# Optimization experiments

Hardware: AMD Instinct MI355X
Metric: run time of the kernel (lower is better)

The kernel has to match this reference:

```python
import jax, jax.numpy as jnp
import numpy as np

H = 200          # GRU hidden size (hard-coded in module)
D = 300          # embed_dim
V = 50000        # embed_num (vocab)
DOC_TRUNC = 10
N_DOCS = 256
T = 50           # words per sentence


def _p(k, shape):
    return jax.random.normal(k, shape, dtype=jnp.float32) * 0.05


def setup_inputs():
    key = jax.random.key(0)
    ks = jax.random.split(key, 24)
    x = jax.random.randint(ks[0], (N_DOCS * DOC_TRUNC, T), 0, V, dtype=jnp.int32)
    doc_lens = jax.random.randint(ks[1], (N_DOCS,), 0, DOC_TRUNC + 1, dtype=jnp.int32)
    emb = _p(ks[2], (V, D)).at[0].set(0.0)  # padding_idx=0 row is zero
    inp = dict(
        x=x, doc_nums=N_DOCS, doc_lens=doc_lens, emb=emb,
        wf_ih=_p(ks[3], (3 * H, D)), wf_hh=_p(ks[4], (3 * H, H)), wf_bi=_p(ks[5], (3 * H,)), wf_bh=_p(ks[6], (3 * H,)),
        wb_ih=_p(ks[7], (3 * H, D)), wb_hh=_p(ks[8], (3 * H, H)), wb_bi=_p(ks[9], (3 * H,)), wb_bh=_p(ks[10], (3 * H,)),
        sf_ih=_p(ks[11], (3 * H, 2 * H)), sf_hh=_p(ks[12], (3 * H, H)), sf_bi=_p(ks[13], (3 * H,)), sf_bh=_p(ks[14], (3 * H,)),
        sb_ih=_p(ks[15], (3 * H, 2 * H)), sb_hh=_p(ks[16], (3 * H, H)), sb_bi=_p(ks[17], (3 * H,)), sb_bh=_p(ks[18], (3 * H,)),
        doc_w=_p(ks[19], (1, 2 * H)), doc_b=_p(ks[20], (1,)),
        sent_w=_p(ks[21], (DOC_TRUNC, 2 * H)), sent_b=_p(ks[22], (DOC_TRUNC,)),
    )
    return inp


def _gru_dir(xseq, w_ih, w_hh, b_ih, b_hh, reverse=False):
    # xseq: [B, T, Din] -> outputs [B, T, H], torch GRU gate order (r, z, n)
    if reverse:
        xseq = xseq[:, ::-1]
    gx = jnp.einsum('btd,gd->btg', xseq, w_ih) + b_ih  # [B, T, 3H]
    gx = jnp.moveaxis(gx, 1, 0)                        # [T, B, 3H]
    h0 = jnp.zeros((xseq.shape[0], H), xseq.dtype)

    def step(h, gxt):
        gh = h @ w_hh.T + b_hh
        xr, xz, xn = jnp.split(gxt, 3, axis=-1)
        hr, hz, hn = jnp.split(gh, 3, axis=-1)
        r = jax.nn.sigmoid(xr + hr)
        z = jax.nn.sigmoid(xz + hz)
        n = jnp.tanh(xn + r * hn)
        h_new = (1.0 - z) * n + z * h
        return h_new, h_new

    _, hs = jax.lax.scan(step, h0, gx)
    hs = jnp.moveaxis(hs, 0, 1)  # [B, T, H]
    if reverse:
        hs = hs[:, ::-1]
    return hs


def _bigru(xseq, fw, bw):
    return jnp.concatenate([_gru_dir(xseq, *fw), _gru_dir(xseq, *bw, reverse=True)], axis=-1)


def _avg_pool(xseq, lens):
    # Faithful to max_pool1d helper: avg over first lens[i] timesteps, zeros if len==0.
    Tn = xseq.shape[1]
    mask = (jnp.arange(Tn)[None, :] < lens[:, None]).astype(xseq.dtype)  # [B, T]
    s = jnp.einsum('btf,bt->bf', xseq, mask)
    denom = jnp.maximum(lens, 1).astype(xseq.dtype)[:, None]
    return jnp.where((lens == 0)[:, None], jnp.zeros_like(s), s / denom)


def reference(x, doc_nums, doc_lens, emb,
              wf_ih, wf_hh, wf_bi, wf_bh, wb_ih, wb_hh, wb_bi, wb_bh,
              sf_ih, sf_hh, sf_bi, sf_bh, sb_ih, sb_hh, sb_bi, sb_bh,
              doc_w, doc_b, sent_w, sent_b):
    sent_lens = jnp.sum(jnp.sign(x), axis=1)                 # [B_sent]
    e = emb[x]                                               # [B_sent, T, D]
    hw = _bigru(e, (wf_ih, wf_hh, wf_bi, wf_bh), (wb_ih, wb_hh, wb_bi, wb_bh))  # [B_sent, T, 2H]
    s = _avg_pool(hw, sent_lens)                             # [B_sent, 2H]
    s = s.reshape(-1, DOC_TRUNC, 2 * H)                      # [N_docs, doc_trunc, 2H]
    hs = _bigru(s, (sf_ih, sf_hh, sf_bi, sf_bh), (sb_ih, sb_hh, sb_bi, sb_bh))  # [N_docs, doc_trunc, 2H]
    d = _avg_pool(hs, doc_lens)                              # [N_docs, 2H]
    doc_pro = (d @ doc_w.T + doc_b).reshape(-1)              # [N_docs]
    sent_pro = d @ sent_w.T + sent_b                         # [N_docs, doc_trunc]
    dl = np.asarray(doc_lens)                                # concrete index data (static)
    rows = np.repeat(np.arange(dl.shape[0]), dl)
    cols = np.concatenate([np.arange(int(l)) for l in dl]).astype(np.int32) if rows.size else np.zeros((0,), np.int32)
    target = jnp.concatenate([doc_pro, sent_pro[rows, cols]])
    return jax.nn.sigmoid(target)
```

## Files before the change

kernel.cpp:

```cpp
#include <hip/hip_runtime.h>
#include <hip/hip_bf16.h>


typedef __hip_bfloat16 bf16;
typedef _Float16 h16x8 __attribute__((ext_vector_type(8)));
typedef __fp16 fp16x2 __attribute__((ext_vector_type(2)));
typedef float f32x4 __attribute__((ext_vector_type(4)));

#define HDIM 200
#define NS   2560
#define TW   50
#define ND   256
#define DTR  10
#define VEMB 50000

#define GT   13
#define NT   39
#define NTP  40
#define KCH  7
#define HSTR 232
#define KC_W 10
#define KC_S 13

__device__ __forceinline__ float sigf(float x) {
    return __builtin_amdgcn_rcpf(1.f + __expf(-x));
}
__device__ __forceinline__ float tanh_fast(float x) {
    float e = __expf(2.f * x);
    return (e - 1.f) * __builtin_amdgcn_rcpf(e + 1.f);
}
__device__ __forceinline__ unsigned short f2h(float x) {
    union { _Float16 h; unsigned short u; } v;
    v.h = (_Float16)x;
    return v.u;
}
__device__ __forceinline__ float h2f(unsigned short u) {
    union { _Float16 h; unsigned short u; } v;
    v.u = u;
    return (float)v.h;
}
__device__ __forceinline__ unsigned pk2h(float a, float b) {
    union { fp16x2 p; unsigned u; } v;
    v.p = __builtin_amdgcn_cvt_pkrtz(a, b);
    return v.u;
}
__device__ __forceinline__ float hfsel(uint2 v, int rg) {
    unsigned u = (rg & 2) ? v.y : v.x;
    return h2f((unsigned short)((rg & 1) ? (u >> 16) : (u & 0xFFFFu)));
}

#define PB_EMBH 12500
#define PB_WHH  (PB_EMBH + 273)
#define PB_BIH  (PB_WHH + 460)
#define PB_ALL  (PB_BIH + 20)

__global__ void prepack_all(
    const float* __restrict__ emb, unsigned short* __restrict__ embH,
    const float* __restrict__ whh0, const float* __restrict__ whh1,
    const float* __restrict__ whh2, const float* __restrict__ whh3,
    unsigned short* __restrict__ Bhh,
    const float* __restrict__ wih0, const float* __restrict__ wih1,
    const float* __restrict__ wih2, const float* __restrict__ wih3,
    unsigned short* __restrict__ BiW0, unsigned short* __restrict__ BiW1,
    unsigned short* __restrict__ BiS0, unsigned short* __restrict__ BiS1,
    const int* __restrict__ x, int* __restrict__ sl,
    const float* bi0, const float* bh0, const float* bi1, const float* bh1,
    const float* bi2, const float* bh2, const float* bi3, const float* bh3,
    float* __restrict__ bt)
{
    const int b = blockIdx.x;
    const int tid = threadIdx.x;

    if (b < PB_EMBH) {
        int gid = b * 256 + tid;
        int row = gid >> 6, c = gid & 63;
        if (c >= 40) return;
        int k0 = c * 8;
        unsigned short vals[8] __attribute__((aligned(16)));
        if (k0 + 7 < 300) {
            const float4 f0 = *reinterpret_cast<const float4*>(emb + (size_t)row * 300 + k0);
            const float4 f1 = *reinterpret_cast<const float4*>(emb + (size_t)row * 300 + k0 + 4);
            unsigned u0 = pk2h(f0.x, f0.y), u1 = pk2h(f0.z, f0.w);
            unsigned u2 = pk2h(f1.x, f1.y), u3 = pk2h(f1.z, f1.w);
            vals[0] = (unsigned short)u0; vals[1] = (unsigned short)(u0 >> 16);
            vals[2] = (unsigned short)u1; vals[3] = (unsigned short)(u1 >> 16);
            vals[4] = (unsigned short)u2; vals[5] = (unsigned short)(u2 >> 16);
            vals[6] = (unsigned short)u3; vals[7] = (unsigned short)(u3 >> 16);
        } else {
#pragma unroll
            for (int jj = 0; jj < 8; ++jj) {
                int k = k0 + jj;
                vals[jj] = (k < 300) ? f2h(emb[(size_t)row * 300 + k]) : (unsigned short)0;
            }
        }
        *reinterpret_cast<uint4*>(embH + (size_t)row * 320 + k0) =
            *reinterpret_cast<const uint4*>(vals);
        return;
    }

    if (b < PB_WHH) {
        int gid = (b - PB_EMBH) * 256 + tid;
        if (gid >= 4 * NT * KCH * 64) return;
        int lane = gid & 63;
        int f = gid >> 6;
        int kc = f % KCH;
        int tIdx = (f / KCH) % NT;
        int d = f / (KCH * NT);
        const float* w = (d == 0) ? whh0 : (d == 1) ? whh1 : (d == 2) ? whh2 : whh3;
        int g = tIdx / GT, j = tIdx % GT;
        int il = j * 16 + (lane & 15);
        int n = g * HDIM + il;
        int kb = kc * 32 + (lane >> 4) * 8;
        unsigned short vals[8] __attribute__((aligned(16)));
#pragma unroll
        for (int jj = 0; jj < 8; ++jj) {
            int k = kb + jj;
            float v = (il < HDIM && k < HDIM) ? w[n * HDIM + k] : 0.f;
            vals[jj] = f2h(v);
        }
        *reinterpret_cast<float4*>(reinterpret_cast<char*>(Bhh) + (size_t)gid * 16) =
            *reinterpret_cast<const float4*>(vals);
        return;
    }

    if (b < PB_BIH) {
        int rel = b - PB_WHH;
        const float* w; unsigned short* Bp; int Kin, KC, base;
        if (rel < 100)      { w = wih0; Bp = BiW0; Kin = 300; KC = KC_W; base = 0; }
        else if (rel < 200) { w = wih1; Bp = BiW1; Kin = 300; KC = KC_W; base = 100; }
        else if (rel < 330) { w = wih2; Bp = BiS0; Kin = 400; KC = KC_S; base = 200; }
        else                { w = wih3; Bp = BiS1; Kin = 400; KC = KC_S; base = 330; }
        int gid = (rel - base) * 256 + tid;
        if (gid >= NTP * KC * 64) return;
        int lane = gid & 63;
        int f = gid >> 6;
        int kc = f % KC;
        int tIdx = f / KC;
        int g = tIdx / GT, j = tIdx % GT;
        int il = j * 16 + (lane & 15);
        int n = g * HDIM + il;
        int kb = kc * 32 + (lane >> 4) * 8;
        unsigned short vals[8] __attribute__((aligned(16)));
#pragma unroll
        for (int jj = 0; jj < 8; ++jj) {
            int k = kb + jj;
            float v = (tIdx < NT && il < HDIM && k < Kin) ? w[n * Kin + k] : 0.f;
            vals[jj] = f2h(v);
        }
        *reinterpret_cast<float4*>(reinterpret_cast<char*>(Bp) + (size_t)gid * 16) =
            *reinterpret_cast<const float4*>(vals);
        return;
    }

    {
        int gid = (b - PB_BIH) * 256 + tid;
        if (gid < NS) {
            int c = 0;
            for (int t = 0; t < TW; ++t) c += (x[gid * TW + t] != 0) ? 1 : 0;
            sl[gid] = c;
            return;
        }
        int g2 = gid - NS;
        if (g2 >= 4 * 624) return;
        int d = g2 / 624, col = g2 % 624;
        int g = col / 208, i = col % 208;
        const float* bi = (d == 0) ? bi0 : (d == 1) ? bi1 : (d == 2) ? bi2 : bi3;
        const float* bh = (d == 0) ? bh0 : (d == 1) ? bh1 : (d == 2) ? bh2 : bh3;
        float v = 0.f;
        if (i < HDIM) v = (g < 2) ? (bi[g * HDIM + i] + bh[g * HDIM + i]) : bi[2 * HDIM + i];
        bt[g2] = v;
    }
}

__global__ __launch_bounds__(512, 2) void gemm_word_fused(
    const unsigned short* __restrict__ embH, const int* __restrict__ idx,
    const unsigned short* __restrict__ Bp0, const unsigned short* __restrict__ Bp1,
    const float* __restrict__ bt0, const float* __restrict__ bt1,
    unsigned short* __restrict__ gx0, unsigned short* __restrict__ gx1,
    int nF, int t0F, int t0B)
{
    __shared__ __align__(16) unsigned short As[128 * 320];

    const int tid = threadIdx.x;
    const int wv = tid >> 6, lane = tid & 63;
    const int d = (blockIdx.x >= nF) ? 1 : 0;
    const int bm = d ? (blockIdx.x - nF) : blockIdx.x;
    const unsigned short* Bp = d ? Bp1 : Bp0;
    const float* bt = d ? bt1 : bt0;
    unsigned short* gxOut = d ? gx1 : gx0;
    const int t0 = d ? t0B : t0F;
    const int m_w = wv & 1, n_w = wv >> 1;

    {
        const int srow = tid >> 2, qk = tid & 3;
        int rp = bm * 128 + srow;
        int tok = idx[(rp % NS) * TW + (rp / NS) + t0];
        const unsigned short* src = embH + (size_t)tok * 320 + qk * 8;
        uint4 v[KC_W];
#pragma unroll
        for (int kc = 0; kc < KC_W; ++kc)
            v[kc] = *reinterpret_cast<const uint4*>(src + kc * 32);
        const int rx = srow & 7;
        unsigned short* dst = &As[srow * 320];
#pragma unroll
        for (int kc = 0; kc < KC_W; ++kc) {
            int slot = (kc * 4 + qk) ^ rx;
            *reinterpret_cast<uint4*>(dst + slot * 8) = v[kc];
        }
    }
    __syncthreads();

    f32x4 acc[4][10];
#pragma unroll
    for (int i = 0; i < 4; ++i)
#pragma unroll
        for (int j = 0; j < 10; ++j) acc[i][j] = (f32x4){0.f, 0.f, 0.f, 0.f};

    const uint4* bq = reinterpret_cast<const uint4*>(Bp);
    const int q = lane >> 4;
    int abase[4], arx[4];
#pragma unroll
    for (int mt = 0; mt < 4; ++mt) {
        int row = m_w * 64 + mt * 16 + (lane & 15);
        abase[mt] = row * 320;
        arx[mt] = row & 7;
    }

#pragma unroll 2
    for (int kc = 0; kc < KC_W; ++kc) {
        h16x8 ah[4];
#pragma unroll
        for (int mt = 0; mt < 4; ++mt) {
            int slot = (kc * 4 + q) ^ arx[mt];
            ah[mt] = *reinterpret_cast<const h16x8*>(&As[abase[mt] + slot * 8]);
        }
#pragma unroll
        for (int half = 0; half < 2; ++half) {
            uint4 b[5];
#pragma unroll
            for (int j = 0; j < 5; ++j) {
                int gnt = n_w * 10 + half * 5 + j;
                b[j] = bq[(size_t)(gnt * KC_W + kc) * 64 + lane];
            }
#pragma unroll
            for (int mt = 0; mt < 4; ++mt)
#pragma unroll
                for (int j = 0; j < 5; ++j)
                    acc[mt][half * 5 + j] = __builtin_amdgcn_mfma_f32_16x16x32_f16(
                        ah[mt], *reinterpret_cast<const h16x8*>(&b[j]),
                        acc[mt][half * 5 + j], 0, 0, 0);
        }
    }

    float btv[10];
#pragma unroll
    for (int j = 0; j < 10; ++j) {
        int gnt = n_w * 10 + j;
        btv[j] = (gnt < NT) ? bt[gnt * 16 + (lane & 15)] : 0.f;
    }

#pragma unroll
    for (int mt = 0; mt < 4; ++mt) {
        int gmt = bm * 8 + m_w * 4 + mt;
#pragma unroll
        for (int j = 0; j < 10; ++j) {
            int gnt = n_w * 10 + j;
            if (gnt < NT) {
                uint2 v;
                v.x = pk2h(acc[mt][j][0] + btv[j], acc[mt][j][1] + btv[j]);
                v.y = pk2h(acc[mt][j][2] + btv[j], acc[mt][j][3] + btv[j]);
                *reinterpret_cast<uint2*>(reinterpret_cast<char*>(gxOut) +
                    ((size_t)(gmt * NT + gnt) * 64 + lane) * 8) = v;
            }
        }
    }
}

__global__ __launch_bounds__(512, 2) void gemm_sent(
    const float* __restrict__ Afl, int astride,
    const unsigned short* __restrict__ Bp0, const unsigned short* __restrict__ Bp1,
    const float* __restrict__ bt0, const float* __restrict__ bt1,
    unsigned short* __restrict__ gx0, unsigned short* __restrict__ gx1, int nF)
{
    __shared__ __align__(16) unsigned short As[2][128 * 32];

    const int tid = threadIdx.x;
    const int wv = tid >> 6, lane = tid & 63;
    const int d = (blockIdx.x >= nF) ? 1 : 0;
    const int bm = d ? (blockIdx.x - nF) : blockIdx.x;
    const unsigned short* Bp = d ? Bp1 : Bp0;
    const float* bt = d ? bt1 : bt0;
    unsigned short* gxOut = d ? gx1 : gx0;
    const int m_w = wv & 1, n_w = wv >> 1;

    int aaddr[4];
#pragma unroll
    for (int mt = 0; mt < 4; ++mt) {
        int row = m_w * 64 + mt * 16 + (lane & 15);
        aaddr[mt] = row * 32 + (((lane >> 4) ^ ((row >> 1) & 3)) << 3);
    }

    const int srow = tid >> 2, qk = tid & 3;
    const int ssw = (srow >> 1) & 3;

    f32x4 acc[4][10];
#pragma unroll
    for (int i = 0; i < 4; ++i)
#pragma unroll
        for (int j = 0; j < 10; ++j) acc[i][j] = (f32x4){0.f, 0.f, 0.f, 0.f};

    const uint4* bq = reinterpret_cast<const uint4*>(Bp);
    const float* arow = Afl + (size_t)(bm * 128 + srow) * astride + qk * 8;

    float4 f[2], fn[2];
#pragma unroll
    for (int j = 0; j < 2; ++j)
        f[j] = *reinterpret_cast<const float4*>(arow + j * 4);

    for (int kc = 0; kc < KC_S; ++kc) {
        unsigned short* Ab = &As[kc & 1][0];
        {
            uint4 vh;
            vh.x = pk2h(f[0].x, f[0].y);
            vh.y = pk2h(f[0].z, f[0].w);
            vh.z = pk2h(f[1].x, f[1].y);
            vh.w = pk2h(f[1].z, f[1].w);
            int slot = qk ^ ssw;
            *reinterpret_cast<uint4*>(&Ab[srow * 32 + slot * 8]) = vh;
        }
        __syncthreads();

        if (kc + 1 < KC_S) {
#pragma unroll
            for (int j = 0; j < 2; ++j)
                fn[j] = *reinterpret_cast<const float4*>(arow + (kc + 1) * 32 + j * 4);
        }

        h16x8 ah[4];
#pragma unroll
        for (int mt = 0; mt < 4; ++mt)
            ah[mt] = *reinterpret_cast<const h16x8*>(&Ab[aaddr[mt]]);

#pragma unroll
        for (int half = 0; half < 2; ++half) {
            uint4 b[5];
#pragma unroll
            for (int j = 0; j < 5; ++j) {
                int gnt = n_w * 10 + half * 5 + j;
                b[j] = bq[(size_t)(gnt * KC_S + kc) * 64 + lane];
            }
#pragma unroll
            for (int mt = 0; mt < 4; ++mt)
#pragma unroll
                for (int j = 0; j < 5; ++j)
                    acc[mt][half * 5 + j] = __builtin_amdgcn_mfma_f32_16x16x32_f16(
                        ah[mt], *reinterpret_cast<const h16x8*>(&b[j]),
                        acc[mt][half * 5 + j], 0, 0, 0);
        }
        if (kc + 1 < KC_S) { f[0] = fn[0]; f[1] = fn[1]; }
    }

    float btv[10];
#pragma unroll
    for (int j = 0; j < 10; ++j) {
        int gnt = n_w * 10 + j;
        btv[j] = (gnt < NT) ? bt[gnt * 16 + (lane & 15)] : 0.f;
    }

#pragma unroll
    for (int mt = 0; mt < 4; ++mt) {
        int gmt = bm * 8 + m_w * 4 + mt;
#pragma unroll
        for (int j = 0; j < 10; ++j) {
            int gnt = n_w * 10 + j;
            if (gnt < NT) {
                uint2 v;
                v.x = pk2h(acc[mt][j][0] + btv[j], acc[mt][j][1] + btv[j]);
                v.y = pk2h(acc[mt][j][2] + btv[j], acc[mt][j][3] + btv[j]);
                *reinterpret_cast<uint2*>(reinterpret_cast<char*>(gxOut) +
                    ((size_t)(gmt * NT + gnt) * 64 + lane) * 8) = v;
            }
        }
    }
}

__global__ __launch_bounds__(832) void gru_fused(
    const unsigned short* __restrict__ gxA, const unsigned short* __restrict__ gxB,
    const unsigned short* __restrict__ Bp, int dirBase0, int dirBase1,
    const float* __restrict__ bh0, const float* __restrict__ bh1,
    const int* __restrict__ lens, float* __restrict__ pool,
    int S, int T, int tSteps, int t0A, int t0B, int poolMode, int nF,
    int first, int last, unsigned short* __restrict__ hstate)
{
    __shared__ __align__(16) unsigned short hh[2][16 * HSTR];

    const int dsel = (blockIdx.x >= nF) ? 1 : 0;
    const int lb = dsel ? (blockIdx.x - nF) : blockIdx.x;
    const unsigned short* gx = dsel ? gxB : gxA;
    const int dirBase = dsel ? dirBase1 : dirBase0;
    const float* bh = dsel ? bh1 : bh0;
    const int dirOff = dsel ? HDIM : 0;
    const int rev = dsel;
    const int t0 = dsel ? t0B : t0A;

    const int tid = threadIdx.x;
    const int w = tid >> 6, lane = tid & 63;
    const int quad = lane >> 4, c = lane & 15;
    const int row0 = lb * 16;
    const int i = w * 16 + c;
    const bool iv = (i < HDIM);

    for (int p = tid; p < 16 * HSTR; p += 832) { hh[0][p] = 0; hh[1][p] = 0; }
    __syncthreads();

    const float bhn = iv ? bh[2 * HDIM + i] : 0.f;

    int slen[4];
    float hreg[4], pacc[4];
#pragma unroll
    for (int rg = 0; rg < 4; ++rg) {
        int L = lens[row0 + quad * 4 + rg];
        if (L < 0) L = 0;
        if (L > T) L = T;
        slen[rg] = L;
        hreg[rg] = 0.f; pacc[rg] = 0.f;
    }

    if (!first && iv) {
#pragma unroll
        for (int rg = 0; rg < 4; ++rg) {
            int sg = row0 + quad * 4 + rg;
            unsigned short hu = hstate[((size_t)dsel * NS + sg) * HDIM + i];
            hreg[rg] = h2f(hu);
            hh[0][(quad * 4 + rg) * HSTR + i] = hu;
        }
    }

    const float4* Bq = reinterpret_cast<const float4*>(Bp);
    h16x8 bfr[3][7];
#pragma unroll
    for (int g = 0; g < 3; ++g)
#pragma unroll
        for (int kc = 0; kc < KCH; ++kc) {
            int fidx = (dirBase + g * GT + w) * KCH + kc;
            float4 raw = Bq[(size_t)fidx * 64 + lane];
            bfr[g][kc] = *reinterpret_cast<h16x8*>(&raw);
        }

    const char* gxb = reinterpret_cast<const char*>(gx);
    const int am = c * HSTR + quad * 8;
    const int SG = S >> 4;
    const int hw0 = (quad * 4) * HSTR + i;
    const long long dstep = (long long)(rev ? -SG : SG) * NT * 512;
    __syncthreads();

    uint2 gxv[3], gnx[3];
    long long goff[3];
    {
        const int tl0 = rev ? (tSteps - 1) : 0;
        const long long gg = (long long)tl0 * SG + lb;
#pragma unroll
        for (int g = 0; g < 3; ++g) {
            long long off = ((gg * NT + g * GT + w) * 64 + lane) * 8;
            gxv[g] = *reinterpret_cast<const uint2*>(gxb + off);
            goff[g] = off + dstep;
        }
    }

    for (int ts = 0; ts < tSteps; ++ts) {
        const int t = rev ? (t0 + tSteps - 1 - ts) : (t0 + ts);
        const int cur = ts & 1, nxt = cur ^ 1;

        if (ts + 1 < tSteps) {
#pragma unroll
            for (int g = 0; g < 3; ++g) {
                gnx[g] = *reinterpret_cast<const uint2*>(gxb + goff[g]);
                goff[g] += dstep;
            }
        }

        f32x4 a0 = (f32x4){0.f, 0.f, 0.f, 0.f}, a1 = a0, a2 = a0;
#pragma unroll
        for (int kc = 0; kc < KCH; ++kc) {
            h16x8 ah = *reinterpret_cast<const h16x8*>(&hh[cur][am + kc * 32]);
            a0 = __builtin_amdgcn_mfma_f32_16x16x32_f16(ah, bfr[0][kc], a0, 0, 0, 0);
            a1 = __builtin_amdgcn_mfma_f32_16x16x32_f16(ah, bfr[1][kc], a1, 0, 0, 0);
            a2 = __builtin_amdgcn_mfma_f32_16x16x32_f16(ah, bfr[2][kc], a2, 0, 0, 0);
        }

        if (iv) {
#pragma unroll
            for (int rg = 0; rg < 4; ++rg) {
                float xr = hfsel(gxv[0], rg);
                float xz = hfsel(gxv[1], rg);
                float xn = hfsel(gxv[2], rg);
                float r = sigf(xr + a0[rg]);
                float z = sigf(xz + a1[rg]);
                float n = tanh_fast(xn + r * (a2[rg] + bhn));
                float hnew = n + z * (hreg[rg] - n);
                hreg[rg] = hnew;
                hh[nxt][hw0 + rg * HSTR] = f2h(hnew);
                pacc[rg] += (t < slen[rg]) ? hnew : 0.f;
            }
        }
        __syncthreads();
        if (ts + 1 < tSteps) {
#pragma unroll
            for (int g = 0; g < 3; ++g) gxv[g] = gnx[g];
        }
    }

    if (iv) {
#pragma unroll
        for (int rg = 0; rg < 4; ++rg) {
            int sg = row0 + quad * 4 + rg;
            if (!last) hstate[((size_t)dsel * NS + sg) * HDIM + i] = f2h(hreg[rg]);
            int L = slen[rg];
            float v = (L > 0) ? pacc[rg] / (float)L : 0.f;
            int prow = poolMode ? ((sg % 10) * ND + sg / 10) : sg;
            float* pp = &pool[(size_t)prow * 400 + dirOff + i];
            if (first) *pp = v; else *pp += v;
        }
    }
}

__global__ __launch_bounds__(64) void head_kernel(
    const float* __restrict__ d_pool, const int* __restrict__ doc_lens,
    const float* __restrict__ doc_w, const float* __restrict__ doc_b,
    const float* __restrict__ sent_w, const float* __restrict__ sent_b,
    float* __restrict__ out)
{
    const int d = blockIdx.x;
    const int lane = threadIdx.x;

    int part = 0;
#pragma unroll
    for (int rep = 0; rep < 4; ++rep) {
        int j = lane + rep * 64;
        int v = doc_lens[j];
        v = (v < 0) ? 0 : (v > DTR ? DTR : v);
        if (j < d) part += v;
    }
#pragma unroll
    for (int off = 32; off; off >>= 1) part += __shfl_down(part, off);
    int soff = __shfl(part, 0);

    int dl = doc_lens[d];
    dl = (dl < 0) ? 0 : (dl > DTR ? DTR : dl);
    const float* dv = d_pool + (size_t)d * 400;

    for (int o = 0; o <= dl; ++o) {
        const float* wrow = (o == 0) ? doc_w : sent_w + (o - 1) * 400;
        float s = 0.f;
        for (int f = lane; f < 400; f += 64) s += dv[f] * wrow[f];
#pragma unroll
        for (int off = 32; off; off >>= 1) s += __shfl_down(s, off);
        if (lane == 0) {
            float bias = (o == 0) ? doc_b[0] : sent_b[o - 1];
            out[(o == 0) ? d : (ND + soff + (o - 1))] = sigf(s + bias);
        }
    }
}

extern "C" void kernel_launch(void* const* d_in, const int* in_sizes, int n_in,
                              void* d_out, int out_size, void* d_ws, size_t ws_size,
                              hipStream_t stream) {
    const int*   x        = (const int*)d_in[0];
    const int*   doc_lens = (const int*)d_in[2];
    const float* emb      = (const float*)d_in[3];
    const float* wf_ih = (const float*)d_in[4];
    const float* wf_hh = (const float*)d_in[5];
    const float* wf_bi = (const float*)d_in[6];
    const float* wf_bh = (const float*)d_in[7];
    const float* wb_ih = (const float*)d_in[8];
    const float* wb_hh = (const float*)d_in[9];
    const float* wb_bi = (const float*)d_in[10];
    const float* wb_bh = (const float*)d_in[11];
    const float* sf_ih = (const float*)d_in[12];
    const float* sf_hh = (const float*)d_in[13];
    const float* sf_bi = (const float*)d_in[14];
    const float* sf_bh = (const float*)d_in[15];
    const float* sb_ih = (const float*)d_in[16];
    const float* sb_hh = (const float*)d_in[17];
    const float* sb_bi = (const float*)d_in[18];
    const float* sb_bh = (const float*)d_in[19];
    const float* doc_w  = (const float*)d_in[20];
    const float* doc_b  = (const float*)d_in[21];
    const float* sent_w = (const float*)d_in[22];
    const float* sent_b = (const float*)d_in[23];

    const size_t GXSZ   = 159744000;
    const size_t GXHALF = 79872000;
    const size_t HSSZ   = 2048000;
    char* ws = (char*)d_ws;
    const size_t base = GXSZ;
    const bool chunked = (ws_size == 0) || (ws_size >= base + 39528448 + HSSZ);

    unsigned short* gxF = (unsigned short*)(ws);
    unsigned short* gxB = (unsigned short*)(ws + GXHALF);
    unsigned short* gxS0 = (unsigned short*)(ws);
    unsigned short* gxS1 = (unsigned short*)(ws + 8000000);
    float* s_in   = (float*)(ws + base);
    float* dpool  = (float*)(ws + base + 4096256);
    int*   sl     = (int*)(ws + base + 4096256 + 409600);
    unsigned short* Bhh  = (unsigned short*)(ws + base + 4096256 + 409600 + 10240);
    unsigned short* BiW0 = (unsigned short*)((char*)Bhh + 1118208);
    unsigned short* BiW1 = BiW0 + NTP * KC_W * 64 * 8;
    unsigned short* BiS0 = (unsigned short*)((char*)BiW0 + 819200);
    unsigned short* BiS1 = BiS0 + NTP * KC_S * 64 * 8;
    float* bt     = (float*)((char*)BiS0 + 1064960);
    unsigned short* embH = (unsigned short*)((char*)bt + 9984);
    unsigned short* hstate = (unsigned short*)(ws + base + 39528448);

    prepack_all<<<PB_ALL, 256, 0, stream>>>(
        emb, embH,
        wf_hh, wb_hh, sf_hh, sb_hh, Bhh,
        wf_ih, wb_ih, sf_ih, sb_ih, BiW0, BiW1, BiS0, BiS1,
        x, sl,
        wf_bi, wf_bh, wb_bi, wb_bh, sf_bi, sf_bh, sb_bi, sb_bh, bt);

    if (chunked) {
        gemm_word_fused<<<1000, 512, 0, stream>>>(
            embH, x, BiW0, BiW1, bt + 0, bt + 624, gxF, gxB, 500, 0, 25);
        gru_fused<<<320, 832, 0, stream>>>(
            gxF, gxB, Bhh, 0 * NT, 1 * NT, wf_bh, wb_bh, sl, s_in,
            NS, TW, 25, 0, 25, 1, 160, 1, 0, hstate);
        gemm_word_fused<<<1000, 512, 0, stream>>>(
            embH, x, BiW0, BiW1, bt + 0, bt + 624, gxF, gxB, 500, 25, 0);
        gru_fused<<<320, 832, 0, stream>>>(
            gxF, gxB, Bhh, 0 * NT, 1 * NT, wf_bh, wb_bh, sl, s_in,
            NS, TW, 25, 25, 0, 1, 160, 0, 1, hstate);
    } else {
        gemm_word_fused<<<1000, 512, 0, stream>>>(
            embH, x, BiW0, BiW1, bt + 0, bt + 624, gxF, gxF, 1000, 0, 0);
        gru_fused<<<160, 832, 0, stream>>>(
            gxF, gxF, Bhh, 0 * NT, 1 * NT, wf_bh, wb_bh, sl, s_in,
            NS, TW, TW, 0, 0, 1, 160, 1, 1, hstate);
        gemm_word_fused<<<1000, 512, 0, stream>>>(
            embH, x, BiW0, BiW1, bt + 0, bt + 624, gxF, gxF, 0, 0, 0);
        gru_fused<<<160, 832, 0, stream>>>(
            gxF, gxF, Bhh, 0 * NT, 1 * NT, wf_bh, wb_bh, sl, s_in,
            NS, TW, TW, 0, 0, 1, 0, 1, 1, hstate);
    }

    gemm_sent<<<40, 512, 0, stream>>>(
        s_in, 400, BiS0, BiS1, bt + 2 * 624, bt + 3 * 624, gxS0, gxS1, 20);
    gru_fused<<<32, 832, 0, stream>>>(
        gxS0, gxS1, Bhh, 2 * NT, 3 * NT, sf_bh, sb_bh, doc_lens, dpool,
        ND, DTR, DTR, 0, 0, 0, 16, 1, 1, hstate);

    head_kernel<<<ND, 64, 0, stream>>>(dpool, doc_lens, doc_w, doc_b, sent_w, sent_b, (float*)d_out);
}
```

Before: 669.3 us.

## Drop time-chunked word GRU path and hstate carry; use int offsets

Removes the two-chunk word-level schedule, which ran two half-length projection GEMMs, each followed by a GRU launch running both directions. It also removes the fp16 hidden-state save and restore between chunks. Instead, one full-length GEMM and 50-step GRU run for the forward direction, then again for the backward direction. The GRU kernel loses its chunk parameters, writes the pool directly, switches gx addressing from 64-bit to 32-bit offsets, and asks for a minimum of 4 blocks per CU in launch bounds. This removes the hidden-state traffic and read-modify-write pooling, but serialises the two directions and doubles the per-launch recurrence length. The tighter launch bound also risks register spills.

```diff
diff --git a/kernel.cpp b/kernel.cpp
--- a/kernel.cpp
+++ b/kernel.cpp
@@ -384,13 +384,12 @@
     }
 }
 
-__global__ __launch_bounds__(832) void gru_fused(
+__global__ __launch_bounds__(832, 4) void gru_fused(
     const unsigned short* __restrict__ gxA, const unsigned short* __restrict__ gxB,
     const unsigned short* __restrict__ Bp, int dirBase0, int dirBase1,
     const float* __restrict__ bh0, const float* __restrict__ bh1,
     const int* __restrict__ lens, float* __restrict__ pool,
-    int S, int T, int tSteps, int t0A, int t0B, int poolMode, int nF,
-    int first, int last, unsigned short* __restrict__ hstate)
+    int S, int T, int poolMode, int nF)
 {
     __shared__ __align__(16) unsigned short hh[2][16 * HSTR];
 
@@ -401,7 +400,6 @@
     const float* bh = dsel ? bh1 : bh0;
     const int dirOff = dsel ? HDIM : 0;
     const int rev = dsel;
-    const int t0 = dsel ? t0B : t0A;
 
     const int tid = threadIdx.x;
     const int w = tid >> 6, lane = tid & 63;
@@ -426,16 +424,6 @@
         hreg[rg] = 0.f; pacc[rg] = 0.f;
     }
 
-    if (!first && iv) {
-#pragma unroll
-        for (int rg = 0; rg < 4; ++rg) {
-            int sg = row0 + quad * 4 + rg;
-            unsigned short hu = hstate[((size_t)dsel * NS + sg) * HDIM + i];
-            hreg[rg] = h2f(hu);
-            hh[0][(quad * 4 + rg) * HSTR + i] = hu;
-        }
-    }
-
     const float4* Bq = reinterpret_cast<const float4*>(Bp);
     h16x8 bfr[3][7];
 #pragma unroll
@@ -451,32 +439,30 @@
     const int am = c * HSTR + quad * 8;
     const int SG = S >> 4;
     const int hw0 = (quad * 4) * HSTR + i;
-    const long long dstep = (long long)(rev ? -SG : SG) * NT * 512;
+    const int GSTR = GT * 64 * 8;
+    const int dstep = (rev ? -SG : SG) * NT * 512;
     __syncthreads();
 
     uint2 gxv[3], gnx[3];
-    long long goff[3];
+    int boff;
     {
-        const int tl0 = rev ? (tSteps - 1) : 0;
-        const long long gg = (long long)tl0 * SG + lb;
-#pragma unroll
-        for (int g = 0; g < 3; ++g) {
-            long long off = ((gg * NT + g * GT + w) * 64 + lane) * 8;
-            gxv[g] = *reinterpret_cast<const uint2*>(gxb + off);
-            goff[g] = off + dstep;
-        }
-    }
-
-    for (int ts = 0; ts < tSteps; ++ts) {
-        const int t = rev ? (t0 + tSteps - 1 - ts) : (t0 + ts);
+        const int t0 = rev ? (T - 1) : 0;
+        boff = (((t0 * SG + lb) * NT + w) * 64 + lane) * 8;
+#pragma unroll
+        for (int g = 0; g < 3; ++g)
+            gxv[g] = *reinterpret_cast<const uint2*>(gxb + boff + g * GSTR);
+        boff += dstep;
+    }
+
+    for (int ts = 0; ts < T; ++ts) {
+        const int t = rev ? (T - 1 - ts) : ts;
         const int cur = ts & 1, nxt = cur ^ 1;
 
-        if (ts + 1 < tSteps) {
-#pragma unroll
-            for (int g = 0; g < 3; ++g) {
-                gnx[g] = *reinterpret_cast<const uint2*>(gxb + goff[g]);
-                goff[g] += dstep;
-            }
+        if (ts + 1 < T) {
+#pragma unroll
+            for (int g = 0; g < 3; ++g)
+                gnx[g] = *reinterpret_cast<const uint2*>(gxb + boff + g * GSTR);
+            boff += dstep;
         }
 
         f32x4 a0 = (f32x4){0.f, 0.f, 0.f, 0.f}, a1 = a0, a2 = a0;
@@ -504,7 +490,7 @@
             }
         }
         __syncthreads();
-        if (ts + 1 < tSteps) {
+        if (ts + 1 < T) {
 #pragma unroll
             for (int g = 0; g < 3; ++g) gxv[g] = gnx[g];
         }
@@ -514,12 +500,10 @@
 #pragma unroll
         for (int rg = 0; rg < 4; ++rg) {
             int sg = row0 + quad * 4 + rg;
-            if (!last) hstate[((size_t)dsel * NS + sg) * HDIM + i] = f2h(hreg[rg]);
             int L = slen[rg];
             float v = (L > 0) ? pacc[rg] / (float)L : 0.f;
             int prow = poolMode ? ((sg % 10) * ND + sg / 10) : sg;
-            float* pp = &pool[(size_t)prow * 400 + dirOff + i];
-            if (first) *pp = v; else *pp += v;
+            pool[(size_t)prow * 400 + dirOff + i] = v;
         }
     }
 }
@@ -589,15 +573,11 @@
     const float* sent_w = (const float*)d_in[22];
     const float* sent_b = (const float*)d_in[23];
 
-    const size_t GXSZ   = 159744000;
-    const size_t GXHALF = 79872000;
-    const size_t HSSZ   = 2048000;
+    const size_t GXSZ = 159744000;
     char* ws = (char*)d_ws;
     const size_t base = GXSZ;
-    const bool chunked = (ws_size == 0) || (ws_size >= base + 39528448 + HSSZ);
-
-    unsigned short* gxF = (unsigned short*)(ws);
-    unsigned short* gxB = (unsigned short*)(ws + GXHALF);
+
+    unsigned short* gxF  = (unsigned short*)(ws);
     unsigned short* gxS0 = (unsigned short*)(ws);
     unsigned short* gxS1 = (unsigned short*)(ws + 8000000);
     float* s_in   = (float*)(ws + base);
@@ -610,7 +590,6 @@
     unsigned short* BiS1 = BiS0 + NTP * KC_S * 64 * 8;
     float* bt     = (float*)((char*)BiS0 + 1064960);
     unsigned short* embH = (unsigned short*)((char*)bt + 9984);
-    unsigned short* hstate = (unsigned short*)(ws + base + 39528448);
 
     prepack_all<<<PB_ALL, 256, 0, stream>>>(
         emb, embH,
@@ -619,35 +598,19 @@
         x, sl,
         wf_bi, wf_bh, wb_bi, wb_bh, sf_bi, sf_bh, sb_bi, sb_bh, bt);
 
-    if (chunked) {
-        gemm_word_fused<<<1000, 512, 0, stream>>>(
-            embH, x, BiW0, BiW1, bt + 0, bt + 624, gxF, gxB, 500, 0, 25);
-        gru_fused<<<320, 832, 0, stream>>>(
-            gxF, gxB, Bhh, 0 * NT, 1 * NT, wf_bh, wb_bh, sl, s_in,
-            NS, TW, 25, 0, 25, 1, 160, 1, 0, hstate);
-        gemm_word_fused<<<1000, 512, 0, stream>>>(
-            embH, x, BiW0, BiW1, bt + 0, bt + 624, gxF, gxB, 500, 25, 0);
-        gru_fused<<<320, 832, 0, stream>>>(
-            gxF, gxB, Bhh, 0 * NT, 1 * NT, wf_bh, wb_bh, sl, s_in,
-            NS, TW, 25, 25, 0, 1, 160, 0, 1, hstate);
-    } else {
-        gemm_word_fused<<<1000, 512, 0, stream>>>(
-            embH, x, BiW0, BiW1, bt + 0, bt + 624, gxF, gxF, 1000, 0, 0);
-        gru_fused<<<160, 832, 0, stream>>>(
-            gxF, gxF, Bhh, 0 * NT, 1 * NT, wf_bh, wb_bh, sl, s_in,
-            NS, TW, TW, 0, 0, 1, 160, 1, 1, hstate);
-        gemm_word_fused<<<1000, 512, 0, stream>>>(
-            embH, x, BiW0, BiW1, bt + 0, bt + 624, gxF, gxF, 0, 0, 0);
-        gru_fused<<<160, 832, 0, stream>>>(
-            gxF, gxF, Bhh, 0 * NT, 1 * NT, wf_bh, wb_bh, sl, s_in,
-            NS, TW, TW, 0, 0, 1, 0, 1, 1, hstate);
-    }
+    gemm_word_fused<<<1000, 512, 0, stream>>>(
+        embH, x, BiW0, BiW1, bt + 0, bt + 624, gxF, gxF, 1000, 0, 0);
+    gru_fused<<<160, 832, 0, stream>>>(
+        gxF, gxF, Bhh, 0 * NT, 1 * NT, wf_bh, wb_bh, sl, s_in, NS, TW, 1, 160);
+    gemm_word_fused<<<1000, 512, 0, stream>>>(
+        embH, x, BiW0, BiW1, bt + 0, bt + 624, gxF, gxF, 0, 0, 0);
+    gru_fused<<<160, 832, 0, stream>>>(
+        gxF, gxF, Bhh, 0 * NT, 1 * NT, wf_bh, wb_bh, sl, s_in, NS, TW, 1, 0);
 
     gemm_sent<<<40, 512, 0, stream>>>(
         s_in, 400, BiS0, BiS1, bt + 2 * 624, bt + 3 * 624, gxS0, gxS1, 20);
     gru_fused<<<32, 832, 0, stream>>>(
-        gxS0, gxS1, Bhh, 2 * NT, 3 * NT, sf_bh, sb_bh, doc_lens, dpool,
-        ND, DTR, DTR, 0, 0, 0, 16, 1, 1, hstate);
+        gxS0, gxS1, Bhh, 2 * NT, 3 * NT, sf_bh, sb_bh, doc_lens, dpool, ND, DTR, 0, 16);
 
     head_kernel<<<ND, 64, 0, stream>>>(dpool, doc_lens, doc_w, doc_b, sent_w, sent_b, (float*)d_out);
 }
```

Measured after the change: 607.9 us. 9.2% less time.
